# Optimization experiments

Measured on AMD Instinct MI355X. Metric: run time of the kernel, lower is better.

The kernel has to match this reference:

```python
import jax, jax.numpy as jnp
import numpy as np
from jax import lax

ALPHA = 0.9      # membrane decay
THRESH = 1.0     # spike threshold
W_SCALE = 0.3    # weight init scale so spikes actually occur


def setup_inputs() -> dict:
    key = jax.random.key(0)
    k0, k1, k2, k3 = jax.random.split(key, 4)
    B, C, T = 512, 16, 2000
    n_res, n_cls = 1024, 10
    x = jax.random.uniform(k0, (B, C, T), dtype=jnp.float32)
    W_in = jax.random.normal(k1, (n_res, C), dtype=jnp.float32) * W_SCALE
    W_res = jax.random.normal(k2, (n_res, n_res), dtype=jnp.float32) * (W_SCALE / np.sqrt(n_res))
    W_clf = jax.random.normal(k3, (n_cls, n_res), dtype=jnp.float32) * (W_SCALE / np.sqrt(n_res))
    return {"x": x, "W_in": W_in, "W_res": W_res, "W_clf": W_clf}


def reference(x, W_in, W_res, W_clf):
    """LIF reservoir + LIF readout, scanned over T timesteps.

    x: (B, C, T). Returns (spike_counts (B, n_classes), reservoir_spikes_accum (B, n_res)).
    Accumulators are carried in the scan state so no (T, B, n) tensor is materialized.
    """
    B, C, T = x.shape
    n_res = W_res.shape[0]
    n_cls = W_clf.shape[0]
    dt = x.dtype

    def step(carry, x_t):
        v_r, s_r, v_c, acc_cls, acc_res = carry
        # reservoir LIF: leaky integrate input + recurrent spikes, threshold, reset
        v_r = ALPHA * v_r + x_t @ W_in.T + s_r @ W_res.T          # (B, n_res)
        s = (v_r >= THRESH).astype(dt)
        v_r = v_r * (1.0 - s)
        # classifier LIF readout driven by reservoir spikes
        v_c = ALPHA * v_c + s @ W_clf.T                            # (B, n_cls)
        s_c = (v_c >= THRESH).astype(dt)
        v_c = v_c * (1.0 - s_c)
        return (v_r, s, v_c, acc_cls + s_c, acc_res + s), None

    init = (
        jnp.zeros((B, n_res), dt),
        jnp.zeros((B, n_res), dt),
        jnp.zeros((B, n_cls), dt),
        jnp.zeros((B, n_cls), dt),
        jnp.zeros((B, n_res), dt),
    )
    xs = jnp.moveaxis(x, -1, 0)  # (T, B, C)
    (_, _, _, spike_counts, res_accum), _ = lax.scan(step, init, xs)
    return spike_counts, res_accum
```

## Files before the change

### kernel.cpp

```cpp
#include <hip/hip_runtime.h>

#define ALPHA 0.9f
#define THRESH 1.0f
#define BATCH 512
#define CIN 16
#define TSTEPS 2000
#define NRES 1024
#define NCLS 10

#define NGROUP 32
#define BPG 8

typedef int   v4i __attribute__((ext_vector_type(4)));
typedef float v4f __attribute__((ext_vector_type(4)));
typedef short v8s __attribute__((ext_vector_type(8)));

#define SLOTC_OFF  8192
#define ROWMAX_OFF 9216
#define MASK_OFF   16384
#define WQF_OFF    278528
#define WCF_OFF    1327104
#define LDS_BYTES  (131072 + 16*1040 + 1024 + 8192)

__global__ __launch_bounds__(256) void maxabs_kernel(const float* __restrict__ W,
                                                     int n, unsigned* __restrict__ slot) {
    unsigned m = 0u;
    for (int i = blockIdx.x * 256 + threadIdx.x; i < n; i += gridDim.x * 256)
        m = max(m, __float_as_uint(W[i]) & 0x7fffffffu);
#pragma unroll
    for (int off = 32; off >= 1; off >>= 1)
        m = max(m, (unsigned)__shfl_xor((int)m, off, 64));
    if ((threadIdx.x & 63) == 0) atomicMax(slot, m);
}

__global__ __launch_bounds__(256) void rowmax_kernel(const float* __restrict__ W,
                                                     float* __restrict__ rowmax) {
    const int row = blockIdx.x * 4 + ((int)threadIdx.x >> 6);
    const int lane = threadIdx.x & 63;
    float m = 0.f;
    for (int j = lane; j < NRES; j += 64) m = fmaxf(m, fabsf(W[row * NRES + j]));
#pragma unroll
    for (int off = 32; off >= 1; off >>= 1) m = fmaxf(m, __shfl_xor(m, off, 64));
    if (lane == 0) rowmax[row] = m;
}

__global__ __launch_bounds__(256) void quant_res(const float* __restrict__ W,
                                                 const float* __restrict__ rowmax,
                                                 unsigned* __restrict__ dst) {
    const int o4 = blockIdx.x * 256 + threadIdx.x;
    const int bl = o4 >> 15, wv = (o4 >> 12) & 7, kt = (o4 >> 8) & 15;
    const int L = (o4 >> 2) & 63, i0 = (o4 & 3) * 4;
    const int n = bl * 128 + wv * 16 + (L & 15);
    const int k = kt * 64 + (L >> 4) * 16 + i0;
    const float inv = 127.0f / rowmax[n];
    unsigned dw = 0;
#pragma unroll
    for (int j = 0; j < 4; ++j) {
        float q = rintf(W[n * NRES + k + j] * inv);
        q = fminf(fmaxf(q, -127.f), 127.f);
        dw |= ((unsigned)((int)q & 0xff)) << (8 * j);
    }
    dst[o4] = dw;
}

__global__ __launch_bounds__(256) void quant_clf(const float* __restrict__ W,
                                                 const unsigned* __restrict__ slot,
                                                 unsigned* __restrict__ dst) {
    const int o4 = blockIdx.x * 256 + threadIdx.x;
    const int kt = (o4 >> 8) & 15, L = (o4 >> 2) & 63, i0 = (o4 & 3) * 4;
    const int cls = L & 15;
    const int k = kt * 64 + (L >> 4) * 16 + i0;
    const float inv = 127.0f / __uint_as_float(*slot);
    unsigned dw = 0;
    if (cls < NCLS) {
#pragma unroll
        for (int j = 0; j < 4; ++j) {
            float q = rintf(W[cls * NRES + k + j] * inv);
            q = fminf(fmaxf(q, -127.f), 127.f);
            dw |= ((unsigned)((int)q & 0xff)) << (8 * j);
        }
    }
    dst[o4] = dw;
}

__device__ __forceinline__ unsigned short f2bf(float f) {
    unsigned u = __float_as_uint(f);
    return (unsigned short)((u + 0x7fffu + ((u >> 16) & 1u)) >> 16);
}

__device__ __forceinline__ v4i expand16(unsigned m16) {
    unsigned w[4];
#pragma unroll
    for (int d = 0; d < 4; ++d)
        w[d] = (((m16 >> (4 * d)) & 15u) * 0x00204081u) & 0x01010101u;
    return *(v4i*)&w[0];
}

__global__ __launch_bounds__(512, 1) void reservoir_mfma(
    const float* __restrict__ x, const float* __restrict__ W_in,
    unsigned char* __restrict__ ws, float* __restrict__ out)
{
    const int q   = (int)blockIdx.x;
    const int g   = (q & 7) * 4 + ((q >> 3) & 3);
    const int bl  = q >> 5;
    const int tid = (int)threadIdx.x;
    const int L    = tid & 63;
    const int wv   = tid >> 6;
    const int col  = L & 15;
    const int rowq = L >> 4;

    extern __shared__ char lds[];
    char* B_lds = lds;
    char* A_lds = lds + 131072;
    unsigned short* xA = (unsigned short*)(lds + 131072 + 16 * 1040);
    char* redC = lds + 131072 + 16 * 1040 + 1024;

    const float* rowmax = (const float*)(ws + ROWMAX_OFF);
    const float cscale = __uint_as_float(*(const unsigned*)(ws + SLOTC_OFF)) * (1.0f / 127.0f);
    unsigned char* maskbuf = ws + MASK_OFF;
    const unsigned char* wqf = ws + WQF_OFF;
    const unsigned char* wcf = ws + WCF_OFF;

    const int nn = bl * 128 + wv * 16 + col;
    const float dscale = rowmax[nn] * (1.0f / 127.0f);
    const bool clfBlk = (bl == 0);

    {
        const v4i* src = (const v4i*)(wqf + (size_t)bl * 131072);
        v4i* dst = (v4i*)B_lds;
        for (int i = tid; i < 8192; i += 512) dst[i] = src[i];
    }

    v8s binf_h, binf_l;
#pragma unroll
    for (int i = 0; i < 8; ++i) {
        const int c = (rowq * 8 + i) & 15;
        const float w = W_in[nn * CIN + c];
        const unsigned short h = f2bf(w);
        const float wl = w - __uint_as_float((unsigned)h << 16);
        binf_h[i] = (short)h;
        binf_l[i] = (short)f2bf(wl);
    }

    v4i bcf0 = {0,0,0,0}, bcf1 = {0,0,0,0};
    if (clfBlk) {
        bcf0 = *(const v4i*)(wcf + (2 * wv + 0) * 1024 + L * 16);
        bcf1 = *(const v4i*)(wcf + (2 * wv + 1) * 1024 + L * 16);
    }

    float v[4]  = {0.f, 0.f, 0.f, 0.f};
    int   accv[4] = {0, 0, 0, 0};
    float vc[4] = {0.f, 0.f, 0.f, 0.f};
    int   accc[4] = {0, 0, 0, 0};

    const int pP = tid >> 3, pk = tid & 7;
    const unsigned long long* mybase0 = (const unsigned long long*)(maskbuf +
        (size_t)(0 * NGROUP + g) * 4096 + pP * 64 + pk * 8);
    const unsigned long long* mybase1 = (const unsigned long long*)(maskbuf +
        (size_t)(1 * NGROUP + g) * 4096 + pP * 64 + pk * 8);

    __syncthreads();

    for (int t = 0; t < TSTEPS; ++t) {
        float xval = 0.f;
        if (tid < 256) {
            const int b = tid >> 4, c = tid & 15;
            xval = x[((size_t)(g * 16 + b) * CIN + c) * TSTEPS + t];
        }

        if (t > 0) {
            const unsigned long long* mp = ((t - 1) & 1) ? mybase1 : mybase0;
            const unsigned want = (unsigned)t;
            unsigned lo, hi;
            for (;;) {
                const unsigned long long u =
                    __hip_atomic_load(mp, __ATOMIC_RELAXED, __HIP_MEMORY_SCOPE_AGENT);
                lo = (unsigned)u; hi = (unsigned)(u >> 32);
                if (((lo >> 16) == want) & ((hi >> 16) == want)) break;
                __builtin_amdgcn_s_sleep(1);
            }
            *(v4i*)(A_lds + (2 * pk + 0) * 1040 + pP * 16) = expand16(lo & 0xffffu);
            *(v4i*)(A_lds + (2 * pk + 1) * 1040 + pP * 16) = expand16(hi & 0xffffu);
        }
        if (tid < 256) {
            const int b = tid >> 4, c = tid & 15;
            const unsigned short h = f2bf(xval);
            const float lo2 = xval - __uint_as_float((unsigned)h << 16);
            xA[b * 32 + c] = h;
            xA[b * 32 + 16 + c] = f2bf(lo2);
        }
        __syncthreads();

        v4f Din;
        {
            const v8s xa = *(const v8s*)((const char*)xA + col * 64 + rowq * 16);
            v4f z = {0.f, 0.f, 0.f, 0.f};
            const v4f D1 = __builtin_amdgcn_mfma_f32_16x16x32_bf16(xa, binf_h, z, 0, 0, 0);
            Din = __builtin_amdgcn_mfma_f32_16x16x32_bf16(xa, binf_l, D1, 0, 0, 0);
        }

        v4i Drec = {0, 0, 0, 0};
        if (t > 0) {
            const char* Bb = B_lds + wv * 16384;
            const char* Ab = A_lds + col * 1040 + rowq * 16;
            v4i Dr0 = {0,0,0,0}, Dr1 = {0,0,0,0};
#pragma unroll 4
            for (int kt = 0; kt < 16; kt += 2) {
                const v4i a0 = *(const v4i*)(Ab + kt * 64);
                const v4i b0 = *(const v4i*)(Bb + kt * 1024 + L * 16);
                const v4i a1 = *(const v4i*)(Ab + (kt + 1) * 64);
                const v4i b1 = *(const v4i*)(Bb + (kt + 1) * 1024 + L * 16);
                Dr0 = __builtin_amdgcn_mfma_i32_16x16x64_i8(a0, b0, Dr0, 0, 0, 0);
                Dr1 = __builtin_amdgcn_mfma_i32_16x16x64_i8(a1, b1, Dr1, 0, 0, 0);
            }
#pragma unroll
            for (int r = 0; r < 4; ++r) Drec[r] = Dr0[r] + Dr1[r];
        }

        unsigned long long bal0, bal1, bal2, bal3;
        {
            float vn; int s;
            vn = ALPHA * v[0] + Din[0] + dscale * (float)Drec[0];
            s = (vn >= THRESH); accv[0] += s; v[0] = s ? 0.f : vn; bal0 = __ballot(s);
            vn = ALPHA * v[1] + Din[1] + dscale * (float)Drec[1];
            s = (vn >= THRESH); accv[1] += s; v[1] = s ? 0.f : vn; bal1 = __ballot(s);
            vn = ALPHA * v[2] + Din[2] + dscale * (float)Drec[2];
            s = (vn >= THRESH); accv[2] += s; v[2] = s ? 0.f : vn; bal2 = __ballot(s);
            vn = ALPHA * v[3] + Din[3] + dscale * (float)Drec[3];
            s = (vn >= THRESH); accv[3] += s; v[3] = s ? 0.f : vn; bal3 = __ballot(s);
        }

        {
            const int p = t & 1;
            if (L < 16) {
                const int b = L;
                const unsigned long long bb = (b & 2) ? ((b & 1) ? bal3 : bal2)
                                                      : ((b & 1) ? bal1 : bal0);
                const unsigned fld = (unsigned)((bb >> ((b >> 2) * 16)) & 0xFFFFu);
                unsigned* mp = (unsigned*)(maskbuf +
                    (size_t)(p * NGROUP + g) * 4096 + (bl * 8 + wv) * 64 + b * 4);
                __hip_atomic_store(mp, ((unsigned)(t + 1) << 16) | fld,
                                   __ATOMIC_RELAXED, __HIP_MEMORY_SCOPE_AGENT);
            }
        }

        if (clfBlk && t > 0) {
            const char* Ab = A_lds + col * 1040 + rowq * 16;
            v4i Dc = {0, 0, 0, 0};
            const v4i a0 = *(const v4i*)(Ab + (2 * wv + 0) * 64);
            const v4i a1 = *(const v4i*)(Ab + (2 * wv + 1) * 64);
            Dc = __builtin_amdgcn_mfma_i32_16x16x64_i8(a0, bcf0, Dc, 0, 0, 0);
            Dc = __builtin_amdgcn_mfma_i32_16x16x64_i8(a1, bcf1, Dc, 0, 0, 0);
            *(v4i*)(redC + wv * 1024 + L * 16) = Dc;
        }
        __syncthreads();

        if (clfBlk && wv == 0 && t > 0) {
            v4i c0 = *(const v4i*)(redC + 0 * 1024 + L * 16);
#pragma unroll
            for (int jj = 1; jj < 8; ++jj) {
                const v4i cj = *(const v4i*)(redC + jj * 1024 + L * 16);
#pragma unroll
                for (int r = 0; r < 4; ++r) c0[r] += cj[r];
            }
#pragma unroll
            for (int r = 0; r < 4; ++r) {
                const float vcn = ALPHA * vc[r] + cscale * (float)c0[r];
                const int sc = (vcn >= THRESH);
                accc[r] += sc;
                vc[r] = sc ? 0.f : vcn;
            }
        }
    }

    if (clfBlk) {
        {
            const unsigned want = (unsigned)TSTEPS;
            unsigned lo, hi;
            for (;;) {
                const unsigned long long u =
                    __hip_atomic_load(mybase1, __ATOMIC_RELAXED, __HIP_MEMORY_SCOPE_AGENT);
                lo = (unsigned)u; hi = (unsigned)(u >> 32);
                if (((lo >> 16) == want) & ((hi >> 16) == want)) break;
                __builtin_amdgcn_s_sleep(1);
            }
            *(v4i*)(A_lds + (2 * pk + 0) * 1040 + pP * 16) = expand16(lo & 0xffffu);
            *(v4i*)(A_lds + (2 * pk + 1) * 1040 + pP * 16) = expand16(hi & 0xffffu);
        }
        __syncthreads();
        {
            const char* Ab = A_lds + col * 1040 + rowq * 16;
            v4i Dc = {0, 0, 0, 0};
            const v4i a0 = *(const v4i*)(Ab + (2 * wv + 0) * 64);
            const v4i a1 = *(const v4i*)(Ab + (2 * wv + 1) * 64);
            Dc = __builtin_amdgcn_mfma_i32_16x16x64_i8(a0, bcf0, Dc, 0, 0, 0);
            Dc = __builtin_amdgcn_mfma_i32_16x16x64_i8(a1, bcf1, Dc, 0, 0, 0);
            *(v4i*)(redC + wv * 1024 + L * 16) = Dc;
        }
        __syncthreads();
        if (wv == 0 && col < NCLS) {
            v4i c0 = *(const v4i*)(redC + 0 * 1024 + L * 16);
#pragma unroll
            for (int jj = 1; jj < 8; ++jj) {
                const v4i cj = *(const v4i*)(redC + jj * 1024 + L * 16);
#pragma unroll
                for (int r = 0; r < 4; ++r) c0[r] += cj[r];
            }
#pragma unroll
            for (int r = 0; r < 4; ++r) {
                const float vcn = ALPHA * vc[r] + cscale * (float)c0[r];
                const int sc = (vcn >= THRESH);
                out[(size_t)(g * 16 + rowq * 4 + r) * NCLS + col] = (float)(accc[r] + sc);
            }
        }
    }
    {
#pragma unroll
        for (int r = 0; r < 4; ++r) {
            const int bglob = g * 16 + rowq * 4 + r;
            out[BATCH * NCLS + (size_t)bglob * NRES + nn] = (float)accv[r];
        }
    }
}

extern "C" void kernel_launch(void* const* d_in, const int* in_sizes, int n_in,
                              void* d_out, int out_size, void* d_ws, size_t ws_size,
                              hipStream_t stream) {
    (void)in_sizes; (void)n_in; (void)out_size; (void)ws_size;
    const float* x     = (const float*)d_in[0];
    const float* W_in  = (const float*)d_in[1];
    const float* W_res = (const float*)d_in[2];
    const float* W_clf = (const float*)d_in[3];
    float* out = (float*)d_out;
    unsigned char* ws = (unsigned char*)d_ws;

    hipMemsetAsync(ws, 0, MASK_OFF + 262144, stream);
    rowmax_kernel<<<256, 256, 0, stream>>>(W_res, (float*)(ws + ROWMAX_OFF));
    maxabs_kernel<<<16, 256, 0, stream>>>(W_clf, NCLS * NRES, (unsigned*)(ws + SLOTC_OFF));
    quant_res<<<1024, 256, 0, stream>>>(W_res, (const float*)(ws + ROWMAX_OFF),
                                        (unsigned*)(ws + WQF_OFF));
    quant_clf<<<16, 256, 0, stream>>>(W_clf, (const unsigned*)(ws + SLOTC_OFF),
                                      (unsigned*)(ws + WCF_OFF));
    reservoir_mfma<<<NGROUP * BPG, 512, LDS_BYTES, stream>>>(x, W_in, ws, out);
}
```

Measured before the change: 3.483 ms.

## Move cross-block spike-mask wait before the barrier and prefetch next input

The spin-wait on the global spike-mask flags for step t+1 now sits at the end of step t, just after the classifier MFMA and before the second barrier, instead of at the top of the next step. Its result is held in registers and expanded into LDS at the start of the next iteration. The x value for the next timestep is also loaded one step ahead, so global latency overlaps with the compute. The aim is to hide the inter-block synchronization and load latency inside the existing barrier window. In exchange, the last iteration now also performs the final wait, and the waiting happens while other waves are still in the barrier phase.

```diff
diff --git a/kernel.cpp b/kernel.cpp
--- a/kernel.cpp
+++ b/kernel.cpp
@@ -159,37 +159,29 @@
     const unsigned long long* mybase1 = (const unsigned long long*)(maskbuf +
         (size_t)(1 * NGROUP + g) * 4096 + pP * 64 + pk * 8);
 
+    const int xb = (tid >> 4) & 15, xc = tid & 15;
+    const size_t xoff = ((size_t)(g * 16 + xb) * CIN + xc) * TSTEPS;
+    float xval = (tid < 256) ? x[xoff] : 0.f;
+
+    unsigned plo = 0, phi = 0;
+
     __syncthreads();
 
     for (int t = 0; t < TSTEPS; ++t) {
-        float xval = 0.f;
+        if (t > 0) {
+            *(v4i*)(A_lds + (2 * pk + 0) * 1040 + pP * 16) = expand16(plo & 0xffffu);
+            *(v4i*)(A_lds + (2 * pk + 1) * 1040 + pP * 16) = expand16(phi & 0xffffu);
+        }
         if (tid < 256) {
-            const int b = tid >> 4, c = tid & 15;
-            xval = x[((size_t)(g * 16 + b) * CIN + c) * TSTEPS + t];
-        }
-
-        if (t > 0) {
-            const unsigned long long* mp = ((t - 1) & 1) ? mybase1 : mybase0;
-            const unsigned want = (unsigned)t;
-            unsigned lo, hi;
-            for (;;) {
-                const unsigned long long u =
-                    __hip_atomic_load(mp, __ATOMIC_RELAXED, __HIP_MEMORY_SCOPE_AGENT);
-                lo = (unsigned)u; hi = (unsigned)(u >> 32);
-                if (((lo >> 16) == want) & ((hi >> 16) == want)) break;
-                __builtin_amdgcn_s_sleep(1);
-            }
-            *(v4i*)(A_lds + (2 * pk + 0) * 1040 + pP * 16) = expand16(lo & 0xffffu);
-            *(v4i*)(A_lds + (2 * pk + 1) * 1040 + pP * 16) = expand16(hi & 0xffffu);
-        }
-        if (tid < 256) {
-            const int b = tid >> 4, c = tid & 15;
             const unsigned short h = f2bf(xval);
             const float lo2 = xval - __uint_as_float((unsigned)h << 16);
-            xA[b * 32 + c] = h;
-            xA[b * 32 + 16 + c] = f2bf(lo2);
+            xA[xb * 32 + xc] = h;
+            xA[xb * 32 + 16 + xc] = f2bf(lo2);
         }
         __syncthreads();
+
+        float xnext = 0.f;
+        if (tid < 256 && t + 1 < TSTEPS) xnext = x[xoff + (t + 1)];
 
         v4f Din;
         {
@@ -253,6 +245,18 @@
             Dc = __builtin_amdgcn_mfma_i32_16x16x64_i8(a1, bcf1, Dc, 0, 0, 0);
             *(v4i*)(redC + wv * 1024 + L * 16) = Dc;
         }
+
+        {
+            const unsigned long long* mp = (t & 1) ? mybase1 : mybase0;
+            const unsigned want = (unsigned)(t + 1);
+            for (;;) {
+                const unsigned long long u =
+                    __hip_atomic_load(mp, __ATOMIC_RELAXED, __HIP_MEMORY_SCOPE_AGENT);
+                plo = (unsigned)u; phi = (unsigned)(u >> 32);
+                if (((plo >> 16) == want) & ((phi >> 16) == want)) break;
+                __builtin_amdgcn_s_sleep(1);
+            }
+        }
         __syncthreads();
 
         if (clfBlk && wv == 0 && t > 0) {
@@ -271,22 +275,12 @@
                 vc[r] = sc ? 0.f : vcn;
             }
         }
+        xval = xnext;
     }
 
     if (clfBlk) {
-        {
-            const unsigned want = (unsigned)TSTEPS;
-            unsigned lo, hi;
-            for (;;) {
-                const unsigned long long u =
-                    __hip_atomic_load(mybase1, __ATOMIC_RELAXED, __HIP_MEMORY_SCOPE_AGENT);
-                lo = (unsigned)u; hi = (unsigned)(u >> 32);
-                if (((lo >> 16) == want) & ((hi >> 16) == want)) break;
-                __builtin_amdgcn_s_sleep(1);
-            }
-            *(v4i*)(A_lds + (2 * pk + 0) * 1040 + pP * 16) = expand16(lo & 0xffffu);
-            *(v4i*)(A_lds + (2 * pk + 1) * 1040 + pP * 16) = expand16(hi & 0xffffu);
-        }
+        *(v4i*)(A_lds + (2 * pk + 0) * 1040 + pP * 16) = expand16(plo & 0xffffu);
+        *(v4i*)(A_lds + (2 * pk + 1) * 1040 + pP * 16) = expand16(phi & 0xffffu);
         __syncthreads();
         {
             const char* Ab = A_lds + col * 1040 + rowq * 16;
```

Result: slower. 5.323 ms (+52.8%).
